# Kernel tuning notes

Hardware: AMD Instinct MI355X
Metric: run time of the kernel (lower is better)

Reference implementation:

```python
import jax, jax.numpy as jnp
import numpy as np

B, N, T, D, H, L, N_HOP = 8, 512, 64, 256, 256, 2, 1
NEG = -1e18


def setup_inputs() -> dict:
    key = jax.random.key(0)
    ks = jax.random.split(key, 16)
    sc = 0.05
    return {
        "attn_mem": jax.random.normal(ks[0], (B, N, D), jnp.float32),
        "mem_sizes": jax.random.randint(ks[1], (B,), 1, N + 1).astype(jnp.int32),
        "lstm_in": jax.random.normal(ks[2], (B, T, D), jnp.float32),
        "init_h": jax.random.uniform(ks[3], (L, H), jnp.float32, -0.01, 0.01),
        "init_c": jax.random.uniform(ks[4], (L, H), jnp.float32, -0.01, 0.01),
        "init_i": jax.random.uniform(ks[5], (D,), jnp.float32, -0.1, 0.1),
        # stacked LSTM weights (layer0 input dim D == H so stacking is valid)
        "w_ih": jax.random.normal(ks[6], (L, 4 * H, D), jnp.float32) * sc,
        "w_hh": jax.random.normal(ks[7], (L, 4 * H, H), jnp.float32) * sc,
        "b_ih": jnp.zeros((L, 4 * H), jnp.float32),
        "b_hh": jnp.zeros((L, 4 * H), jnp.float32),
        "attn_wm": jax.random.normal(ks[8], (D, H), jnp.float32) * sc,
        "attn_wq": jax.random.normal(ks[9], (H, H), jnp.float32) * sc,
        "attn_v": jax.random.uniform(ks[10], (H,), jnp.float32, -0.01, 0.01),
        "hop_wm": jax.random.normal(ks[11], (D, H), jnp.float32) * sc,
        "hop_wq": jax.random.normal(ks[12], (H, H), jnp.float32) * sc,
        "hop_v": jax.random.uniform(ks[13], (H,), jnp.float32, -0.01, 0.01),
    }


def _additive_score(feat, query, v, wq):
    # feat: [B,N,H]  query: [B,S,H]  ->  score: [B,S,N]
    q = query @ wq  # [B,S,H]
    s = jnp.tanh(feat[:, None, :, :] + q[:, :, None, :])  # [B,S,N,H] (large)
    return jnp.einsum("bsnh,h->bsn", s, v)


def _run_lstm(x, h0, c0, w_ih, w_hh, b_ih, b_hh):
    # x: [S,B,D] time-major; PyTorch gate order i,f,g,o
    n_layer = h0.shape[0]

    def step(carry, x_t):
        h, c = carry
        inp = x_t
        hs, cs = [], []
        for l in range(n_layer):
            g = inp @ w_ih[l].T + h[l] @ w_hh[l].T + b_ih[l] + b_hh[l]
            i_g, f_g, g_g, o_g = jnp.split(g, 4, axis=-1)
            c_n = jax.nn.sigmoid(f_g) * c[l] + jax.nn.sigmoid(i_g) * jnp.tanh(g_g)
            h_n = jax.nn.sigmoid(o_g) * jnp.tanh(c_n)
            hs.append(h_n)
            cs.append(c_n)
            inp = h_n
        return (jnp.stack(hs), jnp.stack(cs)), inp

    _, ys = jax.lax.scan(step, (h0, c0), x)
    return ys  # [S,B,H]


def reference(attn_mem, mem_sizes, lstm_in, init_h, init_c, init_i,
              w_ih, w_hh, b_ih, b_hh,
              attn_wm, attn_wq, attn_v, hop_wm, hop_wq, hop_v):
    bs, n_mem, _ = attn_mem.shape
    attn_feat = attn_mem @ attn_wm  # [B,N,H]
    hop_feat = attn_mem @ hop_wm    # [B,N,H]

    h0 = jnp.broadcast_to(init_h[:, None, :], (init_h.shape[0], bs, init_h.shape[1]))
    c0 = jnp.broadcast_to(init_c[:, None, :], h0.shape)
    seq = jnp.concatenate(
        [jnp.broadcast_to(init_i[None, None, :], (bs, 1, init_i.shape[0])), lstm_in],
        axis=1,
    )  # [B,T+1,D]
    query = _run_lstm(seq.transpose(1, 0, 2), h0, c0, w_ih, w_hh, b_ih, b_hh)
    query = query.transpose(1, 0, 2)  # [B,T+1,H]

    valid = jnp.arange(n_mem)[None, None, :] < mem_sizes[:, None, None]  # [B,1,N]
    for _ in range(N_HOP):
        score = _additive_score(hop_feat, query, hop_v, hop_wq)  # [B,T+1,N]
        score = jnp.where(valid, score, NEG)
        norm = jax.nn.softmax(score, axis=-1)
        query = jnp.einsum("bsn,bnh->bsh", norm, hop_feat)

    return _additive_score(attn_feat, query, attn_v, attn_wq)  # [B,T+1,N]
```

## Files before the change

### kernel.cpp

```cpp
#include <hip/hip_runtime.h>

#define BB 8
#define NN 512
#define TT 64
#define SS 65
#define DD 256
#define HH 256
#define G4 1024

__device__ __forceinline__ float fsigmoid(float x) {
    return __builtin_amdgcn_rcpf(1.f + __expf(-x));
}
__device__ __forceinline__ float ftanh(float x) {
    float e = __expf(2.f * x);
    return fmaf(-2.f, __builtin_amdgcn_rcpf(e + 1.f), 1.f);
}

__global__ void __launch_bounds__(256) xgprep_kernel(
    const float* __restrict__ lstm_in, const float* __restrict__ init_i,
    const float* __restrict__ init_h, const float* __restrict__ w_ih,
    const float* __restrict__ b_ih, const float* __restrict__ b_hh,
    float* __restrict__ xg0,
    unsigned long long* __restrict__ S0, unsigned long long* __restrict__ S1)
{
    const int tid = threadIdx.x;
    if (blockIdx.x >= 144) {
        int i = (blockIdx.x - 144) * 256 + tid;
        if (i < 2048) {
            S0[i] = (1ULL << 32) | (unsigned long long)(unsigned)__float_as_uint(init_h[i & 255]);
        } else if (i < 4096) {
            S1[i - 2048] = (1ULL << 32)
                         | (unsigned long long)(unsigned)__float_as_uint(init_h[HH + (i & 255)]);
        } else if (i < 4096 + 65 * 2048) {
            S0[2048 + (i - 4096)] = 0ULL;
        } else {
            S1[2048 + (i - (4096 + 65 * 2048))] = 0ULL;
        }
        return;
    }
    __shared__ float As[16][68];
    __shared__ float Bs[16][68];
    const int bm = ((int)blockIdx.x % 9) * 64, bn = ((int)blockIdx.x / 9) * 64;
    const int tm = (tid >> 4) * 4, tn = (tid & 15) * 4;
    const int arow = tid >> 2, akq = (tid & 3) << 2;
    float acc[4][4] = {};
    for (int k0 = 0; k0 < 256; k0 += 16) {
        {
            int m = bm + arow;
            float4 v = make_float4(0.f, 0.f, 0.f, 0.f);
            if (m < 520) {
                int s = m % 65, b = m / 65;
                const float* src = (s == 0) ? (init_i + k0 + akq)
                                            : (lstm_in + ((size_t)b * TT + (s - 1)) * DD + k0 + akq);
                v = *(const float4*)src;
            }
            As[akq + 0][arow] = v.x; As[akq + 1][arow] = v.y;
            As[akq + 2][arow] = v.z; As[akq + 3][arow] = v.w;
        }
        {
            int n = bn + arow;
            float4 v = *(const float4*)(w_ih + (size_t)n * 256 + k0 + akq);
            Bs[akq + 0][n - bn] = v.x; Bs[akq + 1][n - bn] = v.y;
            Bs[akq + 2][n - bn] = v.z; Bs[akq + 3][n - bn] = v.w;
        }
        __syncthreads();
#pragma unroll
        for (int kk = 0; kk < 16; ++kk) {
            float4 a = *(const float4*)&As[kk][tm];
            float4 b = *(const float4*)&Bs[kk][tn];
            float av[4] = {a.x, a.y, a.z, a.w};
            float bv[4] = {b.x, b.y, b.z, b.w};
#pragma unroll
            for (int i = 0; i < 4; ++i)
#pragma unroll
                for (int jj = 0; jj < 4; ++jj)
                    acc[i][jj] = fmaf(av[i], bv[jj], acc[i][jj]);
        }
        __syncthreads();
    }
    float bad[4];
#pragma unroll
    for (int jj = 0; jj < 4; ++jj)
        bad[jj] = b_ih[bn + tn + jj] + b_hh[bn + tn + jj];
#pragma unroll
    for (int i = 0; i < 4; ++i) {
        int m = bm + tm + i;
        if (m < 520)
            *(float4*)(xg0 + (size_t)m * 1024 + bn + tn) =
                make_float4(acc[i][0] + bad[0], acc[i][1] + bad[1],
                            acc[i][2] + bad[2], acc[i][3] + bad[3]);
    }
}

__device__ __forceinline__ float dot16(const float4* w, const float* hp) {
    float4 s = make_float4(0.f, 0.f, 0.f, 0.f);
#pragma unroll
    for (int k = 0; k < 16; ++k) {
        float4 h4 = *(const float4*)(hp + 4 * k);
        s.x = fmaf(w[k].x, h4.x, s.x);
        s.y = fmaf(w[k].y, h4.y, s.y);
        s.z = fmaf(w[k].z, h4.z, s.z);
        s.w = fmaf(w[k].w, h4.w, s.w);
    }
    return (s.x + s.y) + (s.z + s.w);
}

__device__ __forceinline__ void poll2(const unsigned long long* p, unsigned want,
                                      float* d0, float* d1) {
    unsigned long long a = __hip_atomic_load(p,     __ATOMIC_RELAXED, __HIP_MEMORY_SCOPE_AGENT);
    unsigned long long b = __hip_atomic_load(p + 1, __ATOMIC_RELAXED, __HIP_MEMORY_SCOPE_AGENT);
    while ((unsigned)(a >> 32) != want)
        a = __hip_atomic_load(p, __ATOMIC_RELAXED, __HIP_MEMORY_SCOPE_AGENT);
    while ((unsigned)(b >> 32) != want)
        b = __hip_atomic_load(p + 1, __ATOMIC_RELAXED, __HIP_MEMORY_SCOPE_AGENT);
    *d0 = __uint_as_float((unsigned)a);
    *d1 = __uint_as_float((unsigned)b);
}

#define PIN16(w) do { _Pragma("unroll") \
    for (int _k = 0; _k < 16; ++_k) \
        asm volatile("" : "+v"(w[_k].x), "+v"(w[_k].y), "+v"(w[_k].z), "+v"(w[_k].w)); \
} while (0)

__global__ void __launch_bounds__(1024, 4) mega_kernel(
    const float* __restrict__ w_ih, const float* __restrict__ w_hh,
    const float* __restrict__ b_ih, const float* __restrict__ b_hh,
    const float* __restrict__ xg0, const float* __restrict__ init_c,
    unsigned long long* __restrict__ S0, unsigned long long* __restrict__ S1,
    float* __restrict__ query,
    const float* __restrict__ attn_mem, const float* __restrict__ attn_wm,
    const float* __restrict__ hop_wm,
    float* __restrict__ attn_feat, float* __restrict__ hop_feat)
{
    __shared__ float smem[13056];
    const int tid = threadIdx.x;
    const int blk = blockIdx.x;

    if (blk >= 96) {
        const int grp = tid >> 8, tsub = tid & 255;
        const int tileid = (blk - 96) * 4 + grp;
        const int bm = (tileid & 63) * 64, bn = (tileid >> 6) * 64;
        float* As  = smem + grp * 3264;
        float* Bs  = As + 1088;
        float* Bs2 = As + 2176;
        const int tm = (tsub >> 4) * 4, tn = (tsub & 15) * 4;
        const int arow = tsub >> 2, akq = (tsub & 3) << 2;
        float acc1[4][4] = {}, acc2[4][4] = {};
        for (int k0 = 0; k0 < 256; k0 += 16) {
            float4 va = *(const float4*)(attn_mem + (size_t)(bm + arow) * 256 + k0 + akq);
            As[(akq + 0) * 68 + arow] = va.x; As[(akq + 1) * 68 + arow] = va.y;
            As[(akq + 2) * 68 + arow] = va.z; As[(akq + 3) * 68 + arow] = va.w;
            int kk = tsub >> 4, nq = (tsub & 15) << 2;
            *(float4*)&Bs[kk * 68 + nq]  = *(const float4*)(attn_wm + (size_t)(k0 + kk) * 256 + bn + nq);
            *(float4*)&Bs2[kk * 68 + nq] = *(const float4*)(hop_wm  + (size_t)(k0 + kk) * 256 + bn + nq);
            __syncthreads();
#pragma unroll
            for (int kk2 = 0; kk2 < 16; ++kk2) {
                float4 a  = *(const float4*)&As[kk2 * 68 + tm];
                float4 b1 = *(const float4*)&Bs[kk2 * 68 + tn];
                float4 b2 = *(const float4*)&Bs2[kk2 * 68 + tn];
                float av[4] = {a.x, a.y, a.z, a.w};
                float b1v[4] = {b1.x, b1.y, b1.z, b1.w};
                float b2v[4] = {b2.x, b2.y, b2.z, b2.w};
#pragma unroll
                for (int i = 0; i < 4; ++i)
#pragma unroll
                    for (int jj = 0; jj < 4; ++jj) {
                        acc1[i][jj] = fmaf(av[i], b1v[jj], acc1[i][jj]);
                        acc2[i][jj] = fmaf(av[i], b2v[jj], acc2[i][jj]);
                    }
            }
            __syncthreads();
        }
#pragma unroll
        for (int i = 0; i < 4; ++i) {
            int m = bm + tm + i;
            *(float4*)(attn_feat + (size_t)m * 256 + bn + tn) =
                make_float4(acc1[i][0], acc1[i][1], acc1[i][2], acc1[i][3]);
            *(float4*)(hop_feat + (size_t)m * 256 + bn + tn) =
                make_float4(acc2[i][0], acc2[i][1], acc2[i][2], acc2[i][3]);
        }
        return;
    }

    float* hls  = smem;
    float* part = smem + 4352;
    const int g = tid * 2;
    const int sb = g >> 8, r0 = g & 255, sg0 = r0 >> 6, kq = r0 & 63;
    float* const dst = &hls[(sg0 * 8 + sb) * 68 + kq];

    if (blk < 32) {
        const int jl = tid & 7, gate = (tid >> 3) & 3, b = (tid >> 5) & 7, seg = tid >> 8;
        const int j0 = blk * 8, j = j0 + jl;
        float4 w[16];
        {
            const float4* wr = (const float4*)(w_hh + (size_t)(gate * HH + j) * HH + seg * 64);
#pragma unroll
            for (int k = 0; k < 16; ++k) w[k] = wr[k];
        }
        PIN16(w);
        const int fj = tid >> 3, fb = tid & 7;
        float creg = (tid < 64) ? init_c[j0 + fj] : 0.f;
        const int chunk = seg * 8 + b;
        const int pidx = (chunk * 8 + jl) * 4 + gate;

        for (int t = 0; t < SS; ++t) {
            float xg[4];
            if (tid < 64) {
                const float* xp = xg0 + ((size_t)fb * SS + t) * G4 + (j0 + fj);
#pragma unroll
                for (int gg = 0; gg < 4; ++gg) xg[gg] = xp[gg * 256];
            }
            poll2(S0 + (size_t)t * 2048 + g, (unsigned)(t + 1), &dst[0], &dst[1]);
            __syncthreads();
            part[pidx] = dot16(w, &hls[chunk * 68]);
            __syncthreads();
            if (tid < 64) {
                float g0 = xg[0], g1 = xg[1], g2 = xg[2], g3 = xg[3];
#pragma unroll
                for (int s2 = 0; s2 < 4; ++s2) {
                    const float* pp = &part[((s2 * 8 + fb) * 8 + fj) * 4];
                    g0 += pp[0]; g1 += pp[1]; g2 += pp[2]; g3 += pp[3];
                }
                float c = fsigmoid(g1) * creg + fsigmoid(g0) * ftanh(g2);
                float h = fsigmoid(g3) * ftanh(c);
                creg = c;
                unsigned long long u = ((unsigned long long)(unsigned)(t + 2) << 32)
                                     | (unsigned long long)(unsigned)__float_as_uint(h);
                __hip_atomic_store(S0 + (size_t)(t + 1) * 2048 + fb * 256 + (j0 + fj), u,
                                   __ATOMIC_RELAXED, __HIP_MEMORY_SCOPE_AGENT);
            }
        }
    } else {
        const int jl = tid & 3, gate = (tid >> 2) & 3, b = (tid >> 4) & 7, seg = tid >> 7;
        const int j0 = (blk - 32) * 4, j = j0 + jl;
        float4 w[16];
        {
            const float* base = (seg < 4)
                ? (w_ih + (size_t)(G4 + gate * HH + j) * HH + seg * 64)
                : (w_hh + (size_t)(G4 + gate * HH + j) * HH + (seg - 4) * 64);
            const float4* wr = (const float4*)base;
#pragma unroll
            for (int k = 0; k < 16; ++k) w[k] = wr[k];
        }
        PIN16(w);
        const int fj = tid >> 3, fb = tid & 7;
        float creg = 0.f, bias[4] = {0.f, 0.f, 0.f, 0.f};
        if (tid < 32) {
            creg = init_c[HH + j0 + fj];
#pragma unroll
            for (int gg = 0; gg < 4; ++gg)
                bias[gg] = b_ih[G4 + gg * HH + j0 + fj] + b_hh[G4 + gg * HH + j0 + fj];
        }
        const int chunk = seg * 8 + b;
        const int pidx = chunk * 16 + jl * 4 + gate;

        for (int t = 0; t < SS; ++t) {
            poll2(S0 + (size_t)(t + 1) * 2048 + g, (unsigned)(t + 2), &dst[0], &dst[1]);
            __syncthreads();
            if (seg < 4) part[pidx] = dot16(w, &hls[chunk * 68]);
            poll2(S1 + (size_t)t * 2048 + g, (unsigned)(t + 1),
                  &dst[32 * 68], &dst[32 * 68 + 1]);
            __syncthreads();
            if (seg >= 4) part[pidx] = dot16(w, &hls[chunk * 68]);
            __syncthreads();
            if (tid < 32) {
                float g0 = bias[0], g1 = bias[1], g2 = bias[2], g3 = bias[3];
#pragma unroll
                for (int s2 = 0; s2 < 8; ++s2) {
                    const float* pp = &part[(s2 * 8 + fb) * 16 + fj * 4];
                    g0 += pp[0]; g1 += pp[1]; g2 += pp[2]; g3 += pp[3];
                }
                float c = fsigmoid(g1) * creg + fsigmoid(g0) * ftanh(g2);
                float h = fsigmoid(g3) * ftanh(c);
                creg = c;
                int jj = j0 + fj;
                unsigned long long u = ((unsigned long long)(unsigned)(t + 2) << 32)
                                     | (unsigned long long)(unsigned)__float_as_uint(h);
                __hip_atomic_store(S1 + (size_t)(t + 1) * 2048 + fb * 256 + jj, u,
                                   __ATOMIC_RELAXED, __HIP_MEMORY_SCOPE_AGENT);
                query[((size_t)fb * SS + t) * HH + jj] = h;
            }
        }
    }
}

__global__ void __launch_bounds__(256) post_kernel(
    const float* __restrict__ query, const float* __restrict__ hop_wq,
    const float* __restrict__ hop_feat, const float* __restrict__ hop_v,
    const float* __restrict__ attn_wq, const float* __restrict__ attn_feat,
    const float* __restrict__ attn_v, const int* __restrict__ mem_sizes,
    float* __restrict__ out)
{
    const int s = blockIdx.x, b = blockIdx.y, tid = threadIdx.x;
    __shared__ float qa[256];
    __shared__ float qb[256];
    __shared__ float vv[256];
    __shared__ float sc[512];
    __shared__ float red[8];
    const int msize = mem_sizes[b];
    const int lane = tid & 63, wv = tid >> 6;

    qa[tid] = query[((size_t)b * SS + s) * HH + tid];
    vv[tid] = hop_v[tid];
    __syncthreads();
    {
        float a = 0.f;
        const float* wp = hop_wq + tid;
#pragma unroll 4
        for (int h = 0; h < 256; ++h) a = fmaf(qa[h], wp[(size_t)h * 256], a);
        qb[tid] = a;
    }
    __syncthreads();
    {
        float4 q4 = *(const float4*)&qb[lane << 2];
        float4 v4 = *(const float4*)&vv[lane << 2];
        const float* fb = hop_feat + (size_t)b * NN * HH + (lane << 2);
        for (int n = wv; n < msize; n += 4) {
            float4 f4 = *(const float4*)(fb + (size_t)n * HH);
            float a = ftanh(f4.x + q4.x) * v4.x + ftanh(f4.y + q4.y) * v4.y
                    + ftanh(f4.z + q4.z) * v4.z + ftanh(f4.w + q4.w) * v4.w;
#pragma unroll
            for (int off = 32; off; off >>= 1) a += __shfl_xor(a, off, 64);
            if (lane == 0) sc[n] = a;
        }
    }
    __syncthreads();
    {
        float x0 = (tid < msize) ? sc[tid] : -3e38f;
        float x1 = (tid + 256 < msize) ? sc[tid + 256] : -3e38f;
        float m = fmaxf(x0, x1);
#pragma unroll
        for (int off = 32; off; off >>= 1) m = fmaxf(m, __shfl_xor(m, off, 64));
        if (lane == 0) red[wv] = m;
        __syncthreads();
        m = fmaxf(fmaxf(red[0], red[1]), fmaxf(red[2], red[3]));
        float e0 = __expf(x0 - m), e1 = __expf(x1 - m);
        float l = e0 + e1;
#pragma unroll
        for (int off = 32; off; off >>= 1) l += __shfl_xor(l, off, 64);
        if (lane == 0) red[4 + wv] = l;
        __syncthreads();
        float inv = __builtin_amdgcn_rcpf(red[4] + red[5] + red[6] + red[7]);
        sc[tid] = e0 * inv;
        sc[tid + 256] = e1 * inv;
    }
    __syncthreads();
    {
        float a = 0.f;
        const float* fb = hop_feat + (size_t)b * NN * HH + tid;
        int n = 0;
        for (; n + 4 <= msize; n += 4) {
            a = fmaf(sc[n + 0], fb[(size_t)(n + 0) * HH], a);
            a = fmaf(sc[n + 1], fb[(size_t)(n + 1) * HH], a);
            a = fmaf(sc[n + 2], fb[(size_t)(n + 2) * HH], a);
            a = fmaf(sc[n + 3], fb[(size_t)(n + 3) * HH], a);
        }
        for (; n < msize; ++n) a = fmaf(sc[n], fb[(size_t)n * HH], a);
        __syncthreads();
        qa[tid] = a;
    }
    __syncthreads();
    {
        float a = 0.f;
        const float* wp = attn_wq + tid;
#pragma unroll 4
        for (int h = 0; h < 256; ++h) a = fmaf(qa[h], wp[(size_t)h * 256], a);
        qb[tid] = a;
        vv[tid] = attn_v[tid];
    }
    __syncthreads();
    {
        float4 q4 = *(const float4*)&qb[lane << 2];
        float4 v4 = *(const float4*)&vv[lane << 2];
        const float* fb = attn_feat + (size_t)b * NN * HH + (lane << 2);
        float* ob = out + ((size_t)b * SS + s) * NN;
        for (int n = wv; n < NN; n += 4) {
            float4 f4 = *(const float4*)(fb + (size_t)n * HH);
            float a = ftanh(f4.x + q4.x) * v4.x + ftanh(f4.y + q4.y) * v4.y
                    + ftanh(f4.z + q4.z) * v4.z + ftanh(f4.w + q4.w) * v4.w;
#pragma unroll
            for (int off = 32; off; off >>= 1) a += __shfl_xor(a, off, 64);
            if (lane == 0) ob[n] = a;
        }
    }
}

extern "C" void kernel_launch(void* const* d_in, const int* in_sizes, int n_in,
                              void* d_out, int out_size, void* d_ws, size_t ws_size,
                              hipStream_t stream) {
    const float* attn_mem  = (const float*)d_in[0];
    const int*   mem_sizes = (const int*)d_in[1];
    const float* lstm_in   = (const float*)d_in[2];
    const float* init_h    = (const float*)d_in[3];
    const float* init_c    = (const float*)d_in[4];
    const float* init_i    = (const float*)d_in[5];
    const float* w_ih      = (const float*)d_in[6];
    const float* w_hh      = (const float*)d_in[7];
    const float* b_ih      = (const float*)d_in[8];
    const float* b_hh      = (const float*)d_in[9];
    const float* attn_wm   = (const float*)d_in[10];
    const float* attn_wq   = (const float*)d_in[11];
    const float* attn_v    = (const float*)d_in[12];
    const float* hop_wm    = (const float*)d_in[13];
    const float* hop_wq    = (const float*)d_in[14];
    const float* hop_v     = (const float*)d_in[15];
    float* out = (float*)d_out;

    float* ws        = (float*)d_ws;
    float* attn_feat = ws;
    float* hop_feat  = ws + 1048576;
    float* xg0       = ws + 2097152;
    float* query     = ws + 2629632;
    unsigned long long* S0 = (unsigned long long*)(ws + 2762752);
    unsigned long long* S1 = (unsigned long long*)(ws + 3033088);

    xgprep_kernel<<<1200, 256, 0, stream>>>(lstm_in, init_i, init_h, w_ih,
                                            b_ih, b_hh, xg0, S0, S1);
    {
        void* args[] = { (void*)&w_ih, (void*)&w_hh, (void*)&b_ih, (void*)&b_hh,
                         (void*)&xg0, (void*)&init_c, (void*)&S0, (void*)&S1,
                         (void*)&query, (void*)&attn_mem, (void*)&attn_wm,
                         (void*)&hop_wm, (void*)&attn_feat, (void*)&hop_feat };
        hipLaunchCooperativeKernel(mega_kernel, dim3(160), dim3(1024), args, 0u, stream);
    }
    post_kernel<<<dim3(65, 8), 256, 0, stream>>>(query, hop_wq, hop_feat, hop_v,
                                                 attn_wq, attn_feat, attn_v,
                                                 mem_sizes, out);
}
```

Baseline: 354.4 us.

## Restructure pipeline: move feature GEMM to prep, LDS-staged LSTM, batched score kernels

Moves the attn/hop feature GEMMs out of the cooperative LSTM kernel into the prep kernel, so the LSTM kernel runs only 96 recurrent blocks. Those blocks now stage weights in LDS instead of pinning them in registers. The per-(b,s) post kernel is split into a batched query GEMM, a tiled score kernel, a softmax-weighted-sum kernel and a second GEMM/score pass. The score kernel rewrites tanh(f+q) as 1-2/(e^{2f}e^{2q}+1), using precomputed exponentials to cut transcendental work. This adds more launches and intermediate buffers that reuse the semaphore region, and the exp-product form risks overflow for large inputs.

```diff
diff --git a/kernel.cpp b/kernel.cpp
--- a/kernel.cpp
+++ b/kernel.cpp
@@ -16,16 +16,20 @@
     return fmaf(-2.f, __builtin_amdgcn_rcpf(e + 1.f), 1.f);
 }
 
-__global__ void __launch_bounds__(256) xgprep_kernel(
+__global__ void __launch_bounds__(256) pre_kernel(
     const float* __restrict__ lstm_in, const float* __restrict__ init_i,
     const float* __restrict__ init_h, const float* __restrict__ w_ih,
     const float* __restrict__ b_ih, const float* __restrict__ b_hh,
     float* __restrict__ xg0,
+    const float* __restrict__ attn_mem, const float* __restrict__ attn_wm,
+    const float* __restrict__ hop_wm,
+    float* __restrict__ attn_feat, float* __restrict__ hop_feat,
     unsigned long long* __restrict__ S0, unsigned long long* __restrict__ S1)
 {
     const int tid = threadIdx.x;
-    if (blockIdx.x >= 144) {
-        int i = (blockIdx.x - 144) * 256 + tid;
+    const int blk = blockIdx.x;
+    if (blk >= 400) {
+        int i = (blk - 400) * 256 + tid;
         if (i < 2048) {
             S0[i] = (1ULL << 32) | (unsigned long long)(unsigned)__float_as_uint(init_h[i & 255]);
         } else if (i < 4096) {
@@ -33,74 +37,121 @@
                          | (unsigned long long)(unsigned)__float_as_uint(init_h[HH + (i & 255)]);
         } else if (i < 4096 + 65 * 2048) {
             S0[2048 + (i - 4096)] = 0ULL;
-        } else {
+        } else if (i < 4096 + 130 * 2048) {
             S1[2048 + (i - (4096 + 65 * 2048))] = 0ULL;
         }
         return;
     }
-    __shared__ float As[16][68];
-    __shared__ float Bs[16][68];
-    const int bm = ((int)blockIdx.x % 9) * 64, bn = ((int)blockIdx.x / 9) * 64;
+    __shared__ __align__(16) float smem[3264];
     const int tm = (tid >> 4) * 4, tn = (tid & 15) * 4;
     const int arow = tid >> 2, akq = (tid & 3) << 2;
-    float acc[4][4] = {};
-    for (int k0 = 0; k0 < 256; k0 += 16) {
-        {
-            int m = bm + arow;
-            float4 v = make_float4(0.f, 0.f, 0.f, 0.f);
-            if (m < 520) {
-                int s = m % 65, b = m / 65;
-                const float* src = (s == 0) ? (init_i + k0 + akq)
-                                            : (lstm_in + ((size_t)b * TT + (s - 1)) * DD + k0 + akq);
-                v = *(const float4*)src;
-            }
-            As[akq + 0][arow] = v.x; As[akq + 1][arow] = v.y;
-            As[akq + 2][arow] = v.z; As[akq + 3][arow] = v.w;
-        }
-        {
-            int n = bn + arow;
-            float4 v = *(const float4*)(w_ih + (size_t)n * 256 + k0 + akq);
-            Bs[akq + 0][n - bn] = v.x; Bs[akq + 1][n - bn] = v.y;
-            Bs[akq + 2][n - bn] = v.z; Bs[akq + 3][n - bn] = v.w;
-        }
-        __syncthreads();
-#pragma unroll
-        for (int kk = 0; kk < 16; ++kk) {
-            float4 a = *(const float4*)&As[kk][tm];
-            float4 b = *(const float4*)&Bs[kk][tn];
-            float av[4] = {a.x, a.y, a.z, a.w};
-            float bv[4] = {b.x, b.y, b.z, b.w};
-#pragma unroll
-            for (int i = 0; i < 4; ++i)
-#pragma unroll
-                for (int jj = 0; jj < 4; ++jj)
-                    acc[i][jj] = fmaf(av[i], bv[jj], acc[i][jj]);
-        }
-        __syncthreads();
-    }
-    float bad[4];
-#pragma unroll
-    for (int jj = 0; jj < 4; ++jj)
-        bad[jj] = b_ih[bn + tn + jj] + b_hh[bn + tn + jj];
-#pragma unroll
-    for (int i = 0; i < 4; ++i) {
-        int m = bm + tm + i;
-        if (m < 520)
-            *(float4*)(xg0 + (size_t)m * 1024 + bn + tn) =
-                make_float4(acc[i][0] + bad[0], acc[i][1] + bad[1],
-                            acc[i][2] + bad[2], acc[i][3] + bad[3]);
-    }
-}
-
-__device__ __forceinline__ float dot16(const float4* w, const float* hp) {
+
+    if (blk < 144) {
+        float* As = smem;
+        float* Bs = smem + 1088;
+        const int bm = (blk % 9) * 64, bn = (blk / 9) * 64;
+        float acc[4][4] = {};
+        for (int k0 = 0; k0 < 256; k0 += 16) {
+            {
+                int m = bm + arow;
+                float4 v = make_float4(0.f, 0.f, 0.f, 0.f);
+                if (m < 520) {
+                    int s = m % 65, b = m / 65;
+                    const float* src = (s == 0) ? (init_i + k0 + akq)
+                        : (lstm_in + ((size_t)b * TT + (s - 1)) * DD + k0 + akq);
+                    v = *(const float4*)src;
+                }
+                As[(akq + 0) * 68 + arow] = v.x; As[(akq + 1) * 68 + arow] = v.y;
+                As[(akq + 2) * 68 + arow] = v.z; As[(akq + 3) * 68 + arow] = v.w;
+            }
+            {
+                int n = bn + arow;
+                float4 v = *(const float4*)(w_ih + (size_t)n * 256 + k0 + akq);
+                Bs[(akq + 0) * 68 + (n - bn)] = v.x; Bs[(akq + 1) * 68 + (n - bn)] = v.y;
+                Bs[(akq + 2) * 68 + (n - bn)] = v.z; Bs[(akq + 3) * 68 + (n - bn)] = v.w;
+            }
+            __syncthreads();
+#pragma unroll
+            for (int kk = 0; kk < 16; ++kk) {
+                float4 a = *(const float4*)&As[kk * 68 + tm];
+                float4 b = *(const float4*)&Bs[kk * 68 + tn];
+                float av[4] = {a.x, a.y, a.z, a.w};
+                float bv[4] = {b.x, b.y, b.z, b.w};
+#pragma unroll
+                for (int i = 0; i < 4; ++i)
+#pragma unroll
+                    for (int jj = 0; jj < 4; ++jj)
+                        acc[i][jj] = fmaf(av[i], bv[jj], acc[i][jj]);
+            }
+            __syncthreads();
+        }
+        float bad[4];
+#pragma unroll
+        for (int jj = 0; jj < 4; ++jj)
+            bad[jj] = b_ih[bn + tn + jj] + b_hh[bn + tn + jj];
+#pragma unroll
+        for (int i = 0; i < 4; ++i) {
+            int m = bm + tm + i;
+            if (m < 520)
+                *(float4*)(xg0 + (size_t)m * 1024 + bn + tn) =
+                    make_float4(acc[i][0] + bad[0], acc[i][1] + bad[1],
+                                acc[i][2] + bad[2], acc[i][3] + bad[3]);
+        }
+    } else {
+        float* As  = smem;
+        float* Bs  = smem + 1088;
+        float* Bs2 = smem + 2176;
+        const int tileid = blk - 144;
+        const int bm = (tileid & 63) * 64, bn = (tileid >> 6) * 64;
+        float acc1[4][4] = {}, acc2[4][4] = {};
+        for (int k0 = 0; k0 < 256; k0 += 16) {
+            float4 va = *(const float4*)(attn_mem + (size_t)(bm + arow) * 256 + k0 + akq);
+            As[(akq + 0) * 68 + arow] = va.x; As[(akq + 1) * 68 + arow] = va.y;
+            As[(akq + 2) * 68 + arow] = va.z; As[(akq + 3) * 68 + arow] = va.w;
+            int kk = tid >> 4, nq = (tid & 15) << 2;
+            *(float4*)&Bs[kk * 68 + nq]  = *(const float4*)(attn_wm + (size_t)(k0 + kk) * 256 + bn + nq);
+            *(float4*)&Bs2[kk * 68 + nq] = *(const float4*)(hop_wm  + (size_t)(k0 + kk) * 256 + bn + nq);
+            __syncthreads();
+#pragma unroll
+            for (int kk2 = 0; kk2 < 16; ++kk2) {
+                float4 a  = *(const float4*)&As[kk2 * 68 + tm];
+                float4 b1 = *(const float4*)&Bs[kk2 * 68 + tn];
+                float4 b2 = *(const float4*)&Bs2[kk2 * 68 + tn];
+                float av[4] = {a.x, a.y, a.z, a.w};
+                float b1v[4] = {b1.x, b1.y, b1.z, b1.w};
+                float b2v[4] = {b2.x, b2.y, b2.z, b2.w};
+#pragma unroll
+                for (int i = 0; i < 4; ++i)
+#pragma unroll
+                    for (int jj = 0; jj < 4; ++jj) {
+                        acc1[i][jj] = fmaf(av[i], b1v[jj], acc1[i][jj]);
+                        acc2[i][jj] = fmaf(av[i], b2v[jj], acc2[i][jj]);
+                    }
+            }
+            __syncthreads();
+        }
+#pragma unroll
+        for (int i = 0; i < 4; ++i) {
+            int m = bm + tm + i;
+            *(float4*)(attn_feat + (size_t)m * 256 + bn + tn) =
+                make_float4(acc1[i][0], acc1[i][1], acc1[i][2], acc1[i][3]);
+            *(float4*)(hop_feat + (size_t)m * 256 + bn + tn) =
+                make_float4(acc2[i][0], acc2[i][1], acc2[i][2], acc2[i][3]);
+        }
+    }
+}
+
+__device__ __forceinline__ float dot16(const float4* __restrict__ w,
+                                       const float4* __restrict__ hp) {
     float4 s = make_float4(0.f, 0.f, 0.f, 0.f);
 #pragma unroll
     for (int k = 0; k < 16; ++k) {
-        float4 h4 = *(const float4*)(hp + 4 * k);
-        s.x = fmaf(w[k].x, h4.x, s.x);
-        s.y = fmaf(w[k].y, h4.y, s.y);
-        s.z = fmaf(w[k].z, h4.z, s.z);
-        s.w = fmaf(w[k].w, h4.w, s.w);
+        float4 w4 = w[k];
+        float4 h4 = hp[k];
+        s.x = fmaf(w4.x, h4.x, s.x);
+        s.y = fmaf(w4.y, h4.y, s.y);
+        s.z = fmaf(w4.z, h4.z, s.z);
+        s.w = fmaf(w4.w, h4.w, s.w);
     }
     return (s.x + s.y) + (s.z + s.w);
 }
@@ -117,92 +168,47 @@
     *d1 = __uint_as_float((unsigned)b);
 }
 
-#define PIN16(w) do { _Pragma("unroll") \
-    for (int _k = 0; _k < 16; ++_k) \
-        asm volatile("" : "+v"(w[_k].x), "+v"(w[_k].y), "+v"(w[_k].z), "+v"(w[_k].w)); \
-} while (0)
-
-__global__ void __launch_bounds__(1024, 4) mega_kernel(
+__global__ void __launch_bounds__(1024) lstm_kernel(
     const float* __restrict__ w_ih, const float* __restrict__ w_hh,
     const float* __restrict__ b_ih, const float* __restrict__ b_hh,
     const float* __restrict__ xg0, const float* __restrict__ init_c,
     unsigned long long* __restrict__ S0, unsigned long long* __restrict__ S1,
-    float* __restrict__ query,
-    const float* __restrict__ attn_mem, const float* __restrict__ attn_wm,
-    const float* __restrict__ hop_wm,
-    float* __restrict__ attn_feat, float* __restrict__ hop_feat)
+    float* __restrict__ query)
 {
-    __shared__ float smem[13056];
+    __shared__ __align__(16) float wlds[32 * 260];
+    __shared__ __align__(16) float hls[2 * 8 * 260];
+    __shared__ float part[1024];
     const int tid = threadIdx.x;
     const int blk = blockIdx.x;
-
-    if (blk >= 96) {
-        const int grp = tid >> 8, tsub = tid & 255;
-        const int tileid = (blk - 96) * 4 + grp;
-        const int bm = (tileid & 63) * 64, bn = (tileid >> 6) * 64;
-        float* As  = smem + grp * 3264;
-        float* Bs  = As + 1088;
-        float* Bs2 = As + 2176;
-        const int tm = (tsub >> 4) * 4, tn = (tsub & 15) * 4;
-        const int arow = tsub >> 2, akq = (tsub & 3) << 2;
-        float acc1[4][4] = {}, acc2[4][4] = {};
-        for (int k0 = 0; k0 < 256; k0 += 16) {
-            float4 va = *(const float4*)(attn_mem + (size_t)(bm + arow) * 256 + k0 + akq);
-            As[(akq + 0) * 68 + arow] = va.x; As[(akq + 1) * 68 + arow] = va.y;
-            As[(akq + 2) * 68 + arow] = va.z; As[(akq + 3) * 68 + arow] = va.w;
-            int kk = tsub >> 4, nq = (tsub & 15) << 2;
-            *(float4*)&Bs[kk * 68 + nq]  = *(const float4*)(attn_wm + (size_t)(k0 + kk) * 256 + bn + nq);
-            *(float4*)&Bs2[kk * 68 + nq] = *(const float4*)(hop_wm  + (size_t)(k0 + kk) * 256 + bn + nq);
-            __syncthreads();
-#pragma unroll
-            for (int kk2 = 0; kk2 < 16; ++kk2) {
-                float4 a  = *(const float4*)&As[kk2 * 68 + tm];
-                float4 b1 = *(const float4*)&Bs[kk2 * 68 + tn];
-                float4 b2 = *(const float4*)&Bs2[kk2 * 68 + tn];
-                float av[4] = {a.x, a.y, a.z, a.w};
-                float b1v[4] = {b1.x, b1.y, b1.z, b1.w};
-                float b2v[4] = {b2.x, b2.y, b2.z, b2.w};
-#pragma unroll
-                for (int i = 0; i < 4; ++i)
-#pragma unroll
-                    for (int jj = 0; jj < 4; ++jj) {
-                        acc1[i][jj] = fmaf(av[i], b1v[jj], acc1[i][jj]);
-                        acc2[i][jj] = fmaf(av[i], b2v[jj], acc2[i][jj]);
-                    }
-            }
-            __syncthreads();
-        }
-#pragma unroll
-        for (int i = 0; i < 4; ++i) {
-            int m = bm + tm + i;
-            *(float4*)(attn_feat + (size_t)m * 256 + bn + tn) =
-                make_float4(acc1[i][0], acc1[i][1], acc1[i][2], acc1[i][3]);
-            *(float4*)(hop_feat + (size_t)m * 256 + bn + tn) =
-                make_float4(acc2[i][0], acc2[i][1], acc2[i][2], acc2[i][3]);
-        }
-        return;
-    }
-
-    float* hls  = smem;
-    float* part = smem + 4352;
+    const bool is1 = blk >= 32;
+    const int j0 = is1 ? (blk - 32) * 4 : blk * 8;
+
+    if (!is1) {
+        for (int idx = tid; idx < 8192; idx += 1024) {
+            int r = idx >> 8, h = idx & 255;
+            int gate = r >> 3, jl = r & 7;
+            wlds[r * 260 + h] = w_hh[((size_t)(gate * HH + j0 + jl)) * HH + h];
+        }
+    } else {
+        for (int idx = tid; idx < 8192; idx += 1024) {
+            int r = idx >> 8, h = idx & 255;
+            int half = r >> 4, gate = (r >> 2) & 3, jl = r & 3;
+            const float* src = half ? w_hh : w_ih;
+            wlds[r * 260 + h] = src[((size_t)(G4 + gate * HH + j0 + jl)) * HH + h];
+        }
+    }
     const int g = tid * 2;
-    const int sb = g >> 8, r0 = g & 255, sg0 = r0 >> 6, kq = r0 & 63;
-    float* const dst = &hls[(sg0 * 8 + sb) * 68 + kq];
-
-    if (blk < 32) {
-        const int jl = tid & 7, gate = (tid >> 3) & 3, b = (tid >> 5) & 7, seg = tid >> 8;
-        const int j0 = blk * 8, j = j0 + jl;
-        float4 w[16];
-        {
-            const float4* wr = (const float4*)(w_hh + (size_t)(gate * HH + j) * HH + seg * 64);
-#pragma unroll
-            for (int k = 0; k < 16; ++k) w[k] = wr[k];
-        }
-        PIN16(w);
-        const int fj = tid >> 3, fb = tid & 7;
+    const int bs = g >> 8, hs = g & 255;
+    const int fj = is1 ? (tid >> 3) : (tid >> 3);
+    const int fb = tid & 7;
+
+    if (!is1) {
+        const int b = tid & 7, jl = (tid >> 3) & 7, gate = (tid >> 5) & 3, seg = tid >> 8;
+        const float4* wp = (const float4*)&wlds[(gate * 8 + jl) * 260 + seg * 64];
+        const int pidx = seg * 256 + gate * 64 + jl * 8 + b;
+        float* const dst = &hls[bs * 260 + hs];
+        const float4* hp = (const float4*)&hls[b * 260 + seg * 64];
         float creg = (tid < 64) ? init_c[j0 + fj] : 0.f;
-        const int chunk = seg * 8 + b;
-        const int pidx = (chunk * 8 + jl) * 4 + gate;
 
         for (int t = 0; t < SS; ++t) {
             float xg[4];
@@ -211,16 +217,16 @@
 #pragma unroll
                 for (int gg = 0; gg < 4; ++gg) xg[gg] = xp[gg * 256];
             }
-            poll2(S0 + (size_t)t * 2048 + g, (unsigned)(t + 1), &dst[0], &dst[1]);
-            __syncthreads();
-            part[pidx] = dot16(w, &hls[chunk * 68]);
+            poll2(S0 + (size_t)t * 2048 + g, (unsigned)(t + 1), dst, dst + 1);
+            __syncthreads();
+            part[pidx] = dot16(wp, hp);
             __syncthreads();
             if (tid < 64) {
                 float g0 = xg[0], g1 = xg[1], g2 = xg[2], g3 = xg[3];
 #pragma unroll
                 for (int s2 = 0; s2 < 4; ++s2) {
-                    const float* pp = &part[((s2 * 8 + fb) * 8 + fj) * 4];
-                    g0 += pp[0]; g1 += pp[1]; g2 += pp[2]; g3 += pp[3];
+                    const float* pp = &part[s2 * 256 + fj * 8 + fb];
+                    g0 += pp[0];  g1 += pp[64]; g2 += pp[128]; g3 += pp[192];
                 }
                 float c = fsigmoid(g1) * creg + fsigmoid(g0) * ftanh(g2);
                 float h = fsigmoid(g3) * ftanh(c);
@@ -232,19 +238,13 @@
             }
         }
     } else {
-        const int jl = tid & 3, gate = (tid >> 2) & 3, b = (tid >> 4) & 7, seg = tid >> 7;
-        const int j0 = (blk - 32) * 4, j = j0 + jl;
-        float4 w[16];
-        {
-            const float* base = (seg < 4)
-                ? (w_ih + (size_t)(G4 + gate * HH + j) * HH + seg * 64)
-                : (w_hh + (size_t)(G4 + gate * HH + j) * HH + (seg - 4) * 64);
-            const float4* wr = (const float4*)base;
-#pragma unroll
-            for (int k = 0; k < 16; ++k) w[k] = wr[k];
-        }
-        PIN16(w);
-        const int fj = tid >> 3, fb = tid & 7;
+        const int b = tid & 7, jl = (tid >> 3) & 3, gate = (tid >> 5) & 3;
+        const int half = (tid >> 7) & 1, seg = tid >> 8;
+        const float4* wp = (const float4*)&wlds[(half * 16 + gate * 4 + jl) * 260 + seg * 64];
+        const int pidx = seg * 256 + half * 128 + gate * 32 + jl * 8 + b;
+        float* const dst0 = &hls[bs * 260 + hs];
+        float* const dst1 = &hls[2080 + bs * 260 + hs];
+        const float4* hp = (const float4*)&hls[half * 2080 + b * 260 + seg * 64];
         float creg = 0.f, bias[4] = {0.f, 0.f, 0.f, 0.f};
         if (tid < 32) {
             creg = init_c[HH + j0 + fj];
@@ -252,24 +252,21 @@
             for (int gg = 0; gg < 4; ++gg)
                 bias[gg] = b_ih[G4 + gg * HH + j0 + fj] + b_hh[G4 + gg * HH + j0 + fj];
         }
-        const int chunk = seg * 8 + b;
-        const int pidx = chunk * 16 + jl * 4 + gate;
 
         for (int t = 0; t < SS; ++t) {
-            poll2(S0 + (size_t)(t + 1) * 2048 + g, (unsigned)(t + 2), &dst[0], &dst[1]);
-            __syncthreads();
-            if (seg < 4) part[pidx] = dot16(w, &hls[chunk * 68]);
-            poll2(S1 + (size_t)t * 2048 + g, (unsigned)(t + 1),
-                  &dst[32 * 68], &dst[32 * 68 + 1]);
-            __syncthreads();
-            if (seg >= 4) part[pidx] = dot16(w, &hls[chunk * 68]);
+            poll2(S0 + (size_t)(t + 1) * 2048 + g, (unsigned)(t + 2), dst0, dst0 + 1);
+            __syncthreads();
+            if (half == 0) part[pidx] = dot16(wp, hp);
+            poll2(S1 + (size_t)t * 2048 + g, (unsigned)(t + 1), dst1, dst1 + 1);
+            __syncthreads();
+            if (half == 1) part[pidx] = dot16(wp, hp);
             __syncthreads();
             if (tid < 32) {
                 float g0 = bias[0], g1 = bias[1], g2 = bias[2], g3 = bias[3];
 #pragma unroll
                 for (int s2 = 0; s2 < 8; ++s2) {
-                    const float* pp = &part[(s2 * 8 + fb) * 16 + fj * 4];
-                    g0 += pp[0]; g1 += pp[1]; g2 += pp[2]; g3 += pp[3];
+                    const float* pp = &part[(s2 >> 1) * 256 + (s2 & 1) * 128 + fj * 8 + fb];
+                    g0 += pp[0]; g1 += pp[32]; g2 += pp[64]; g3 += pp[96];
                 }
                 float c = fsigmoid(g1) * creg + fsigmoid(g0) * ftanh(g2);
                 float h = fsigmoid(g3) * ftanh(c);
@@ -285,105 +282,168 @@
     }
 }
 
-__global__ void __launch_bounds__(256) post_kernel(
-    const float* __restrict__ query, const float* __restrict__ hop_wq,
-    const float* __restrict__ hop_feat, const float* __restrict__ hop_v,
-    const float* __restrict__ attn_wq, const float* __restrict__ attn_feat,
-    const float* __restrict__ attn_v, const int* __restrict__ mem_sizes,
-    float* __restrict__ out)
+__global__ void __launch_bounds__(256) gemm_kernel(
+    const float* __restrict__ A, const float* __restrict__ B,
+    float* __restrict__ C, int M, int N, int K)
 {
-    const int s = blockIdx.x, b = blockIdx.y, tid = threadIdx.x;
-    __shared__ float qa[256];
-    __shared__ float qb[256];
-    __shared__ float vv[256];
-    __shared__ float sc[512];
-    __shared__ float red[8];
+    __shared__ __align__(16) float As[16 * 68];
+    __shared__ __align__(16) float Bs[16 * 68];
+    const int tid = threadIdx.x;
+    const int bm = blockIdx.x * 64, bn = blockIdx.y * 64;
+    const int tm = (tid >> 4) * 4, tn = (tid & 15) * 4;
+    const int arow = tid >> 2, akq = (tid & 3) << 2;
+    float acc[4][4] = {};
+    for (int k0 = 0; k0 < K; k0 += 16) {
+        {
+            int m = bm + arow;
+            float4 v = make_float4(0.f, 0.f, 0.f, 0.f);
+            if (m < M) v = *(const float4*)(A + (size_t)m * K + k0 + akq);
+            As[(akq + 0) * 68 + arow] = v.x; As[(akq + 1) * 68 + arow] = v.y;
+            As[(akq + 2) * 68 + arow] = v.z; As[(akq + 3) * 68 + arow] = v.w;
+        }
+        {
+            int kk = tid >> 4, nq = (tid & 15) << 2;
+            *(float4*)&Bs[kk * 68 + nq] = *(const float4*)(B + (size_t)(k0 + kk) * N + bn + nq);
+        }
+        __syncthreads();
+#pragma unroll
+        for (int kk2 = 0; kk2 < 16; ++kk2) {
+            float4 a = *(const float4*)&As[kk2 * 68 + tm];
+            float4 b = *(const float4*)&Bs[kk2 * 68 + tn];
+            float av[4] = {a.x, a.y, a.z, a.w};
+            float bv[4] = {b.x, b.y, b.z, b.w};
+#pragma unroll
+            for (int i = 0; i < 4; ++i)
+#pragma unroll
+                for (int jj = 0; jj < 4; ++jj)
+                    acc[i][jj] = fmaf(av[i], bv[jj], acc[i][jj]);
+        }
+        __syncthreads();
+    }
+#pragma unroll
+    for (int i = 0; i < 4; ++i) {
+        int m = bm + tm + i;
+        if (m < M)
+            *(float4*)(C + (size_t)m * N + bn + tn) =
+                make_float4(acc[i][0], acc[i][1], acc[i][2], acc[i][3]);
+    }
+}
+
+__global__ void __launch_bounds__(256) score2_kernel(
+    const float* __restrict__ feat, const float* __restrict__ qv,
+    const float* __restrict__ v, const int* __restrict__ mem_sizes,
+    float* __restrict__ outp, int masked)
+{
+    const int nt = blockIdx.x, st = blockIdx.y, b = blockIdx.z;
+    const int tid = threadIdx.x;
+    const int n0 = nt * 64, s0 = st * 13;
+    const int msize = masked ? mem_sizes[b] : NN;
+    if (n0 >= msize) return;
+    __shared__ float efls[32 * 261];
+    __shared__ float eqls[13 * 261];
+    __shared__ float vls[256];
+
+    vls[tid] = v[tid];
+    for (int k = 0; k < 13; ++k)
+        eqls[k * 261 + tid] = __expf(2.f * qv[((size_t)b * SS + s0 + k) * HH + tid]);
+    __syncthreads();
+    float vsum = 0.f;
+    {
+        float p0 = 0.f, p1 = 0.f, p2 = 0.f, p3 = 0.f;
+#pragma unroll
+        for (int h = 0; h < 256; h += 4) {
+            p0 += vls[h]; p1 += vls[h + 1]; p2 += vls[h + 2]; p3 += vls[h + 3];
+        }
+        vsum = (p0 + p1) + (p2 + p3);
+    }
+
+    for (int c = 0; c < 2; ++c) {
+        const int nbase = n0 + c * 32;
+        int nrows = msize - nbase; nrows = nrows < 0 ? 0 : (nrows > 32 ? 32 : nrows);
+        __syncthreads();
+        for (int k = 0; k < nrows; ++k)
+            efls[k * 261 + tid] = __expf(2.f * feat[((size_t)b * NN + nbase + k) * HH + tid]);
+        __syncthreads();
+#pragma unroll
+        for (int i = 0; i < 2; ++i) {
+            int p = i * 256 + tid;
+            if (p < 416) {
+                int s = p >> 5, nl = p & 31;
+                if (nl < nrows) {
+                    const float* ef = &efls[nl * 261];
+                    const float* eq = &eqls[s * 261];
+                    float acc = 0.f;
+#pragma unroll 4
+                    for (int h = 0; h < 256; ++h)
+                        acc = fmaf(vls[h],
+                                   __builtin_amdgcn_rcpf(fmaf(ef[h], eq[h], 1.f)),
+                                   acc);
+                    outp[((size_t)b * SS + s0 + s) * NN + (nbase + nl)] =
+                        fmaf(-2.f, acc, vsum);
+                }
+            }
+        }
+    }
+}
+
+__global__ void __launch_bounds__(256) smwsum_kernel(
+    const float* __restrict__ sc, const float* __restrict__ feat,
+    const int* __restrict__ mem_sizes, float* __restrict__ q2raw)
+{
+    const int st = blockIdx.x, b = blockIdx.y;
+    const int tid = threadIdx.x;
+    const int s0 = st * 13;
     const int msize = mem_sizes[b];
+    __shared__ float pls[13 * 520];
+    for (int i = tid; i < 13 * 512; i += 256) {
+        int s = i >> 9, n = i & 511;
+        pls[s * 520 + n] = (n < msize)
+            ? sc[((size_t)b * SS + s0 + s) * NN + n] : -3e38f;
+    }
+    __syncthreads();
     const int lane = tid & 63, wv = tid >> 6;
-
-    qa[tid] = query[((size_t)b * SS + s) * HH + tid];
-    vv[tid] = hop_v[tid];
+    for (int r = wv; r < 13; r += 4) {
+        float x[8];
+        float m = -3e38f;
+#pragma unroll
+        for (int k = 0; k < 8; ++k) {
+            x[k] = pls[r * 520 + lane + 64 * k];
+            m = fmaxf(m, x[k]);
+        }
+#pragma unroll
+        for (int off = 32; off; off >>= 1) m = fmaxf(m, __shfl_xor(m, off, 64));
+        float l = 0.f;
+#pragma unroll
+        for (int k = 0; k < 8; ++k) { x[k] = __expf(x[k] - m); l += x[k]; }
+#pragma unroll
+        for (int off = 32; off; off >>= 1) l += __shfl_xor(l, off, 64);
+        float inv = __builtin_amdgcn_rcpf(l);
+#pragma unroll
+        for (int k = 0; k < 8; ++k) pls[r * 520 + lane + 64 * k] = x[k] * inv;
+    }
     __syncthreads();
-    {
-        float a = 0.f;
-        const float* wp = hop_wq + tid;
-#pragma unroll 4
-        for (int h = 0; h < 256; ++h) a = fmaf(qa[h], wp[(size_t)h * 256], a);
-        qb[tid] = a;
-    }
-    __syncthreads();
-    {
-        float4 q4 = *(const float4*)&qb[lane << 2];
-        float4 v4 = *(const float4*)&vv[lane << 2];
-        const float* fb = hop_feat + (size_t)b * NN * HH + (lane << 2);
-        for (int n = wv; n < msize; n += 4) {
-            float4 f4 = *(const float4*)(fb + (size_t)n * HH);
-            float a = ftanh(f4.x + q4.x) * v4.x + ftanh(f4.y + q4.y) * v4.y
-                    + ftanh(f4.z + q4.z) * v4.z + ftanh(f4.w + q4.w) * v4.w;
-#pragma unroll
-            for (int off = 32; off; off >>= 1) a += __shfl_xor(a, off, 64);
-            if (lane == 0) sc[n] = a;
-        }
-    }
-    __syncthreads();
-    {
-        float x0 = (tid < msize) ? sc[tid] : -3e38f;
-        float x1 = (tid + 256 < msize) ? sc[tid + 256] : -3e38f;
-        float m = fmaxf(x0, x1);
-#pragma unroll
-        for (int off = 32; off; off >>= 1) m = fmaxf(m, __shfl_xor(m, off, 64));
-        if (lane == 0) red[wv] = m;
-        __syncthreads();
-        m = fmaxf(fmaxf(red[0], red[1]), fmaxf(red[2], red[3]));
-        float e0 = __expf(x0 - m), e1 = __expf(x1 - m);
-        float l = e0 + e1;
-#pragma unroll
-        for (int off = 32; off; off >>= 1) l += __shfl_xor(l, off, 64);
-        if (lane == 0) red[4 + wv] = l;
-        __syncthreads();
-        float inv = __builtin_amdgcn_rcpf(red[4] + red[5] + red[6] + red[7]);
-        sc[tid] = e0 * inv;
-        sc[tid + 256] = e1 * inv;
-    }
-    __syncthreads();
-    {
-        float a = 0.f;
-        const float* fb = hop_feat + (size_t)b * NN * HH + tid;
-        int n = 0;
-        for (; n + 4 <= msize; n += 4) {
-            a = fmaf(sc[n + 0], fb[(size_t)(n + 0) * HH], a);
-            a = fmaf(sc[n + 1], fb[(size_t)(n + 1) * HH], a);
-            a = fmaf(sc[n + 2], fb[(size_t)(n + 2) * HH], a);
-            a = fmaf(sc[n + 3], fb[(size_t)(n + 3) * HH], a);
-        }
-        for (; n < msize; ++n) a = fmaf(sc[n], fb[(size_t)n * HH], a);
-        __syncthreads();
-        qa[tid] = a;
-    }
-    __syncthreads();
-    {
-        float a = 0.f;
-        const float* wp = attn_wq + tid;
-#pragma unroll 4
-        for (int h = 0; h < 256; ++h) a = fmaf(qa[h], wp[(size_t)h * 256], a);
-        qb[tid] = a;
-        vv[tid] = attn_v[tid];
-    }
-    __syncthreads();
-    {
-        float4 q4 = *(const float4*)&qb[lane << 2];
-        float4 v4 = *(const float4*)&vv[lane << 2];
-        const float* fb = attn_feat + (size_t)b * NN * HH + (lane << 2);
-        float* ob = out + ((size_t)b * SS + s) * NN;
-        for (int n = wv; n < NN; n += 4) {
-            float4 f4 = *(const float4*)(fb + (size_t)n * HH);
-            float a = ftanh(f4.x + q4.x) * v4.x + ftanh(f4.y + q4.y) * v4.y
-                    + ftanh(f4.z + q4.z) * v4.z + ftanh(f4.w + q4.w) * v4.w;
-#pragma unroll
-            for (int off = 32; off; off >>= 1) a += __shfl_xor(a, off, 64);
-            if (lane == 0) ob[n] = a;
-        }
-    }
+    float acc[13];
+#pragma unroll
+    for (int s = 0; s < 13; ++s) acc[s] = 0.f;
+    const float* fb = feat + (size_t)b * NN * HH + tid;
+    int n = 0;
+    for (; n + 2 <= msize; n += 2) {
+        float f0 = fb[(size_t)n * HH];
+        float f1 = fb[(size_t)(n + 1) * HH];
+#pragma unroll
+        for (int s = 0; s < 13; ++s) {
+            acc[s] = fmaf(pls[s * 520 + n], f0, acc[s]);
+            acc[s] = fmaf(pls[s * 520 + n + 1], f1, acc[s]);
+        }
+    }
+    if (n < msize) {
+        float f0 = fb[(size_t)n * HH];
+#pragma unroll
+        for (int s = 0; s < 13; ++s) acc[s] = fmaf(pls[s * 520 + n], f0, acc[s]);
+    }
+#pragma unroll
+    for (int s = 0; s < 13; ++s)
+        q2raw[((size_t)b * SS + s0 + s) * HH + tid] = acc[s];
 }
 
 extern "C" void kernel_launch(void* const* d_in, const int* in_sizes, int n_in,
@@ -412,19 +472,28 @@
     float* hop_feat  = ws + 1048576;
     float* xg0       = ws + 2097152;
     float* query     = ws + 2629632;
-    unsigned long long* S0 = (unsigned long long*)(ws + 2762752);
-    unsigned long long* S1 = (unsigned long long*)(ws + 3033088);
-
-    xgprep_kernel<<<1200, 256, 0, stream>>>(lstm_in, init_i, init_h, w_ih,
-                                            b_ih, b_hh, xg0, S0, S1);
+    float* region    = ws + 2762752;
+    unsigned long long* S0 = (unsigned long long*)region;
+    unsigned long long* S1 = (unsigned long long*)(region + 270336);
+    float* q1     = region;
+    float* sc     = region + 133120;
+    float* q2raw  = region + 399360;
+    float* q2     = region + 532480;
+
+    pre_kernel<<<1456, 256, 0, stream>>>(lstm_in, init_i, init_h, w_ih, b_ih, b_hh,
+                                         xg0, attn_mem, attn_wm, hop_wm,
+                                         attn_feat, hop_feat, S0, S1);
     {
         void* args[] = { (void*)&w_ih, (void*)&w_hh, (void*)&b_ih, (void*)&b_hh,
                          (void*)&xg0, (void*)&init_c, (void*)&S0, (void*)&S1,
-                         (void*)&query, (void*)&attn_mem, (void*)&attn_wm,
-                         (void*)&hop_wm, (void*)&attn_feat, (void*)&hop_feat };
-        hipLaunchCooperativeKernel(mega_kernel, dim3(160), dim3(1024), args, 0u, stream);
-    }
-    post_kernel<<<dim3(65, 8), 256, 0, stream>>>(query, hop_wq, hop_feat, hop_v,
-                                                 attn_wq, attn_feat, attn_v,
-                                                 mem_sizes, out);
-}
+                         (void*)&query };
+        hipLaunchCooperativeKernel(lstm_kernel, dim3(96), dim3(1024), args, 0u, stream);
+    }
+    gemm_kernel<<<dim3(9, 4), 256, 0, stream>>>(query, hop_wq, q1, 520, 256, 256);
+    score2_kernel<<<dim3(8, 5, 8), 256, 0, stream>>>(hop_feat, q1, hop_v,
+                                                     mem_sizes, sc, 1);
+    smwsum_kernel<<<dim3(5, 8), 256, 0, stream>>>(sc, hop_feat, mem_sizes, q2raw);
+    gemm_kernel<<<dim3(9, 4), 256, 0, stream>>>(q2raw, attn_wq, q2, 520, 256, 256);
+    score2_kernel<<<dim3(8, 5, 8), 256, 0, stream>>>(attn_feat, q2, attn_v,
+                                                     mem_sizes, out, 0);
+}
```

After: 462.1 us. +30.4%, slower.
